# Kernel optimization log

Hardware: AMD Instinct MI355X
Metric: run time of the kernel (lower is better)

Reference implementation:

```python
import jax, jax.numpy as jnp
import numpy as np


def _neighbor_indices(e):
    """Replicates the Python branch ladder: for each position i pick two key/value
    slice indices (k1, k2) based on entropy comparisons with neighbors."""
    S = e.shape[0]
    i = jnp.arange(S)
    e_prev = e[jnp.clip(i - 1, 0, S - 1)]
    e_next = e[jnp.clip(i + 1, 0, S - 1)]
    ge_next = e >= e_next
    ge_prev = e >= e_prev
    le_next = e <= e_next
    le_prev = e <= e_prev
    # branch order matters for ties: check in the same order as the torch code
    c1 = ge_next & ge_prev  # local max  -> (i-1, i+1)
    c2 = le_next & ge_prev  # rising     -> (i-1, i)
    c3 = ge_next & le_prev  # falling    -> (i,   i+1)
    k1 = jnp.where(c1, i - 1, jnp.where(c2, i - 1, jnp.where(c3, i, i)))
    k2 = jnp.where(c1, i + 1, jnp.where(c2, i, jnp.where(c3, i + 1, i)))
    # boundary i == 0: (1,1) if e0 >= e1 else (0,0)
    b0 = jnp.where(e[0] >= e[1], 1, 0)
    k1 = k1.at[0].set(b0)
    k2 = k2.at[0].set(b0)
    # boundary i == S-1: (S-2,S-2) if e[-1] >= e[-2] else (S-1,S-1)
    bL = jnp.where(e[S - 1] >= e[S - 2], S - 2, S - 1)
    k1 = k1.at[S - 1].set(bL)
    k2 = k2.at[S - 1].set(bL)
    return k1, k2


def setup_inputs() -> dict:
    key = jax.random.key(0)
    k1, k2 = jax.random.split(key)
    S, C, H, W = 64, 512, 32, 32
    c5d = jax.random.normal(k1, (S, C, H, W), dtype=jnp.float32)
    entropy_list = jax.random.uniform(k2, (S,), dtype=jnp.float32)
    return {"c5d": c5d, "entropy_list": entropy_list}


def reference(c5d, entropy_list):
    S = c5d.shape[0]
    D = int(np.prod(c5d.shape[1:]))
    k1, k2 = _neighbor_indices(entropy_list)
    idx = jnp.stack([k1, k2], axis=1)              # [S, 2]
    q = c5d.reshape(S, D)                          # [S, D]  one token per slice
    kv = q[idx]                                    # [S, 2, D] gathered neighbor tokens
    scale = 1.0 / jnp.sqrt(jnp.asarray(D, dtype=q.dtype))
    scores = jnp.einsum("sd,skd->sk", q, kv) * scale   # [S, 2]
    attn = jax.nn.softmax(scores, axis=-1)
    out = jnp.einsum("sk,skd->sd", attn, kv)           # [S, D]
    return out.reshape(c5d.shape)
```

## Files before the change

kernel.cpp:

```cpp
#include <hip/hip_runtime.h>
#include <math.h>

#define NSLICE 64
#define DVEC   131072
#define NB     32
#define CHUNK4 (DVEC / NB)
#define TPB    256
#define ITER   (CHUNK4 / TPB)
#define NPAIR  (NSLICE - 1)
#define NTASKA (NPAIR * NB)
#define NTASKB (NSLICE * NB)

typedef float f32x4 __attribute__((ext_vector_type(4)));

__inline__ __device__ void nt_store4(const float4& v, float4* p) {
    __builtin_nontemporal_store(*reinterpret_cast<const f32x4*>(&v),
                                reinterpret_cast<f32x4*>(p));
}

__inline__ __device__ float wave_reduce(float v) {
    #pragma unroll
    for (int off = 32; off > 0; off >>= 1) v += __shfl_down(v, off, 64);
    return v;
}

__inline__ __device__ bool is_c1(const float* __restrict__ ent, int s) {
    if (s < 1 || s > NSLICE - 2) return false;
    const float e = ent[s];
    return (e >= ent[s + 1]) && (e >= ent[s - 1]);
}

__global__ __launch_bounds__(TPB) void cross_kernel(
        const float4* __restrict__ q, const float* __restrict__ ent,
        float* __restrict__ pC) {
    const int task = blockIdx.x;
    const int i = task >> 5;
    const int j = task & 31;

    bool need = is_c1(ent, i) || is_c1(ent, i + 1);
    if (!need) return;

    const float4* qi = q + (size_t)i * DVEC + (size_t)j * CHUNK4 + threadIdx.x;
    const float4* qn = qi + DVEC;
    float c0 = 0.f, c1 = 0.f, c2 = 0.f, c3 = 0.f;
    #pragma unroll
    for (int t = 0; t < ITER; t += 4) {
        float4 a0 = qi[(t+0)*TPB]; float4 a1 = qi[(t+1)*TPB];
        float4 a2 = qi[(t+2)*TPB]; float4 a3 = qi[(t+3)*TPB];
        float4 b0 = qn[(t+0)*TPB]; float4 b1 = qn[(t+1)*TPB];
        float4 b2 = qn[(t+2)*TPB]; float4 b3 = qn[(t+3)*TPB];
        c0 += a0.x*b0.x + a0.y*b0.y + a0.z*b0.z + a0.w*b0.w;
        c1 += a1.x*b1.x + a1.y*b1.y + a1.z*b1.z + a1.w*b1.w;
        c2 += a2.x*b2.x + a2.y*b2.y + a2.z*b2.z + a2.w*b2.w;
        c3 += a3.x*b3.x + a3.y*b3.y + a3.z*b3.z + a3.w*b3.w;
    }
    const float cross = (c0 + c1) + (c2 + c3);

    __shared__ float r_c[TPB / 64];
    const float cw = wave_reduce(cross);
    const int lane = threadIdx.x & 63;
    const int wid  = threadIdx.x >> 6;
    if (lane == 0) r_c[wid] = cw;
    __syncthreads();
    if (threadIdx.x == 0) pC[task] = r_c[0] + r_c[1] + r_c[2] + r_c[3];
}

__global__ __launch_bounds__(TPB) void combine_kernel(
        const float4* __restrict__ q, const float* __restrict__ ent,
        const float* __restrict__ pC, float4* __restrict__ out) {
    const int task = blockIdx.x;
    const int i = task >> 5;
    const int j = task & 31;
    const int tid = threadIdx.x;

    __shared__ float sp[64];

    bool blend = false;
    int src = i;
    if (i == 0) {
        src = (ent[0] >= ent[1]) ? 1 : 0;
    } else if (i == NSLICE - 1) {
        src = (ent[NSLICE-1] >= ent[NSLICE-2]) ? NSLICE-2 : NSLICE-1;
    } else {
        const float ei = ent[i], ep = ent[i-1], en = ent[i+1];
        const bool ge_next = (ei >= en), ge_prev = (ei >= ep);
        if (ge_next && ge_prev) blend = true;
    }

    float4* o = out + (size_t)i * DVEC + (size_t)j * CHUNK4 + tid;

    if (!blend) {
        const float4* qs = q + (size_t)src * DVEC + (size_t)j * CHUNK4 + tid;
        #pragma unroll
        for (int t = 0; t < ITER; t += 8) {
            float4 x0 = qs[(t+0)*TPB]; float4 x1 = qs[(t+1)*TPB];
            float4 x2 = qs[(t+2)*TPB]; float4 x3 = qs[(t+3)*TPB];
            float4 x4 = qs[(t+4)*TPB]; float4 x5 = qs[(t+5)*TPB];
            float4 x6 = qs[(t+6)*TPB]; float4 x7 = qs[(t+7)*TPB];
            nt_store4(x0, &o[(t+0)*TPB]);
            nt_store4(x1, &o[(t+1)*TPB]);
            nt_store4(x2, &o[(t+2)*TPB]);
            nt_store4(x3, &o[(t+3)*TPB]);
            nt_store4(x4, &o[(t+4)*TPB]);
            nt_store4(x5, &o[(t+5)*TPB]);
            nt_store4(x6, &o[(t+6)*TPB]);
            nt_store4(x7, &o[(t+7)*TPB]);
        }
        return;
    }

    if (tid < 64)
        sp[tid] = (tid < 32) ? pC[(i - 1) * NB + tid] : pC[i * NB + (tid - 32)];
    __syncthreads();

    float s1a = 0.f, s2a = 0.f;
    #pragma unroll
    for (int t = 0; t < NB; t++) {
        s1a += sp[t];
        s2a += sp[32 + t];
    }
    const float s_scale = 1.0f / sqrtf(524288.0f);
    const float s1 = s1a * s_scale;
    const float s2 = s2a * s_scale;
    const float m  = fmaxf(s1, s2);
    const float e1 = expf(s1 - m), e2 = expf(s2 - m);
    const float inv = 1.0f / (e1 + e2);
    const float wa = e1 * inv;
    const float wb = e2 * inv;

    const float4* qa = q + (size_t)(i - 1) * DVEC + (size_t)j * CHUNK4 + tid;
    const float4* qb = q + (size_t)(i + 1) * DVEC + (size_t)j * CHUNK4 + tid;
    #pragma unroll
    for (int t = 0; t < ITER; t += 4) {
        float4 x0 = qa[(t+0)*TPB]; float4 x1 = qa[(t+1)*TPB];
        float4 x2 = qa[(t+2)*TPB]; float4 x3 = qa[(t+3)*TPB];
        float4 y0 = qb[(t+0)*TPB]; float4 y1 = qb[(t+1)*TPB];
        float4 y2 = qb[(t+2)*TPB]; float4 y3 = qb[(t+3)*TPB];
        float4 r0, r1, r2, r3;
        r0.x = wa*x0.x + wb*y0.x; r0.y = wa*x0.y + wb*y0.y;
        r0.z = wa*x0.z + wb*y0.z; r0.w = wa*x0.w + wb*y0.w;
        r1.x = wa*x1.x + wb*y1.x; r1.y = wa*x1.y + wb*y1.y;
        r1.z = wa*x1.z + wb*y1.z; r1.w = wa*x1.w + wb*y1.w;
        r2.x = wa*x2.x + wb*y2.x; r2.y = wa*x2.y + wb*y2.y;
        r2.z = wa*x2.z + wb*y2.z; r2.w = wa*x2.w + wb*y2.w;
        r3.x = wa*x3.x + wb*y3.x; r3.y = wa*x3.y + wb*y3.y;
        r3.z = wa*x3.z + wb*y3.z; r3.w = wa*x3.w + wb*y3.w;
        nt_store4(r0, &o[(t+0)*TPB]);
        nt_store4(r1, &o[(t+1)*TPB]);
        nt_store4(r2, &o[(t+2)*TPB]);
        nt_store4(r3, &o[(t+3)*TPB]);
    }
}

extern "C" void kernel_launch(void* const* d_in, const int* in_sizes, int n_in,
                              void* d_out, int out_size, void* d_ws, size_t ws_size,
                              hipStream_t stream) {
    const float4* c5d = (const float4*)d_in[0];
    const float*  ent = (const float*)d_in[1];
    float4* out = (float4*)d_out;

    float* pC = (float*)d_ws;

    cross_kernel<<<NTASKA, TPB, 0, stream>>>(c5d, ent, pC);
    combine_kernel<<<NTASKB, TPB, 0, stream>>>(c5d, ent, pC, out);
}
```

Baseline: 241.8 us.

## Fuse cross and combine kernels into one cooperative launch with grid sync

Replaces the two back-to-back kernel launches with a single cooperative kernel of 1024 blocks. Each block handles up to two cross-product tasks, waits at a grid-wide barrier, then handles two combine tasks. If the cooperative launch fails it falls back to the original two kernels. This removes one launch and the gap between kernels, but adds grid-sync cost and caps residency at 1024 persistent blocks, which may lower memory-level parallelism for the copy-heavy combine phase.

```diff
diff --git a/kernel.cpp b/kernel.cpp
--- a/kernel.cpp
+++ b/kernel.cpp
@@ -1,5 +1,8 @@
 #include <hip/hip_runtime.h>
+#include <hip/hip_cooperative_groups.h>
 #include <math.h>
+
+namespace cg = cooperative_groups;
 
 #define NSLICE 64
 #define DVEC   131072
@@ -10,6 +13,7 @@
 #define NPAIR  (NSLICE - 1)
 #define NTASKA (NPAIR * NB)
 #define NTASKB (NSLICE * NB)
+#define FBLK   1024
 
 typedef float f32x4 __attribute__((ext_vector_type(4)));
 
@@ -30,15 +34,11 @@
     return (e >= ent[s + 1]) && (e >= ent[s - 1]);
 }
 
-__global__ __launch_bounds__(TPB) void cross_kernel(
-        const float4* __restrict__ q, const float* __restrict__ ent,
-        float* __restrict__ pC) {
-    const int task = blockIdx.x;
+__device__ void cross_task(int task, const float4* __restrict__ q,
+                           const float* __restrict__ ent, float* __restrict__ pC) {
     const int i = task >> 5;
     const int j = task & 31;
-
-    bool need = is_c1(ent, i) || is_c1(ent, i + 1);
-    if (!need) return;
+    if (!(is_c1(ent, i) || is_c1(ent, i + 1))) return;
 
     const float4* qi = q + (size_t)i * DVEC + (size_t)j * CHUNK4 + threadIdx.x;
     const float4* qn = qi + DVEC;
@@ -63,17 +63,16 @@
     if (lane == 0) r_c[wid] = cw;
     __syncthreads();
     if (threadIdx.x == 0) pC[task] = r_c[0] + r_c[1] + r_c[2] + r_c[3];
+    __syncthreads();
 }
 
-__global__ __launch_bounds__(TPB) void combine_kernel(
-        const float4* __restrict__ q, const float* __restrict__ ent,
-        const float* __restrict__ pC, float4* __restrict__ out) {
-    const int task = blockIdx.x;
+__device__ void combine_task(int task, const float4* __restrict__ q,
+                             const float* __restrict__ ent,
+                             const float* __restrict__ pC,
+                             float4* __restrict__ out) {
     const int i = task >> 5;
     const int j = task & 31;
     const int tid = threadIdx.x;
-
-    __shared__ float sp[64];
 
     bool blend = false;
     int src = i;
@@ -83,8 +82,7 @@
         src = (ent[NSLICE-1] >= ent[NSLICE-2]) ? NSLICE-2 : NSLICE-1;
     } else {
         const float ei = ent[i], ep = ent[i-1], en = ent[i+1];
-        const bool ge_next = (ei >= en), ge_prev = (ei >= ep);
-        if (ge_next && ge_prev) blend = true;
+        if ((ei >= en) && (ei >= ep)) blend = true;
     }
 
     float4* o = out + (size_t)i * DVEC + (size_t)j * CHUNK4 + tid;
@@ -97,36 +95,29 @@
             float4 x2 = qs[(t+2)*TPB]; float4 x3 = qs[(t+3)*TPB];
             float4 x4 = qs[(t+4)*TPB]; float4 x5 = qs[(t+5)*TPB];
             float4 x6 = qs[(t+6)*TPB]; float4 x7 = qs[(t+7)*TPB];
-            nt_store4(x0, &o[(t+0)*TPB]);
-            nt_store4(x1, &o[(t+1)*TPB]);
-            nt_store4(x2, &o[(t+2)*TPB]);
-            nt_store4(x3, &o[(t+3)*TPB]);
-            nt_store4(x4, &o[(t+4)*TPB]);
-            nt_store4(x5, &o[(t+5)*TPB]);
-            nt_store4(x6, &o[(t+6)*TPB]);
-            nt_store4(x7, &o[(t+7)*TPB]);
+            nt_store4(x0, &o[(t+0)*TPB]); nt_store4(x1, &o[(t+1)*TPB]);
+            nt_store4(x2, &o[(t+2)*TPB]); nt_store4(x3, &o[(t+3)*TPB]);
+            nt_store4(x4, &o[(t+4)*TPB]); nt_store4(x5, &o[(t+5)*TPB]);
+            nt_store4(x6, &o[(t+6)*TPB]); nt_store4(x7, &o[(t+7)*TPB]);
         }
         return;
     }
 
+    __shared__ float sp[64];
     if (tid < 64)
         sp[tid] = (tid < 32) ? pC[(i - 1) * NB + tid] : pC[i * NB + (tid - 32)];
     __syncthreads();
-
     float s1a = 0.f, s2a = 0.f;
     #pragma unroll
-    for (int t = 0; t < NB; t++) {
-        s1a += sp[t];
-        s2a += sp[32 + t];
-    }
+    for (int t = 0; t < NB; t++) { s1a += sp[t]; s2a += sp[32 + t]; }
+    __syncthreads();
+
     const float s_scale = 1.0f / sqrtf(524288.0f);
-    const float s1 = s1a * s_scale;
-    const float s2 = s2a * s_scale;
+    const float s1 = s1a * s_scale, s2 = s2a * s_scale;
     const float m  = fmaxf(s1, s2);
     const float e1 = expf(s1 - m), e2 = expf(s2 - m);
     const float inv = 1.0f / (e1 + e2);
-    const float wa = e1 * inv;
-    const float wb = e2 * inv;
+    const float wa = e1 * inv, wb = e2 * inv;
 
     const float4* qa = q + (size_t)(i - 1) * DVEC + (size_t)j * CHUNK4 + tid;
     const float4* qb = q + (size_t)(i + 1) * DVEC + (size_t)j * CHUNK4 + tid;
@@ -145,11 +136,32 @@
         r2.z = wa*x2.z + wb*y2.z; r2.w = wa*x2.w + wb*y2.w;
         r3.x = wa*x3.x + wb*y3.x; r3.y = wa*x3.y + wb*y3.y;
         r3.z = wa*x3.z + wb*y3.z; r3.w = wa*x3.w + wb*y3.w;
-        nt_store4(r0, &o[(t+0)*TPB]);
-        nt_store4(r1, &o[(t+1)*TPB]);
-        nt_store4(r2, &o[(t+2)*TPB]);
-        nt_store4(r3, &o[(t+3)*TPB]);
+        nt_store4(r0, &o[(t+0)*TPB]); nt_store4(r1, &o[(t+1)*TPB]);
+        nt_store4(r2, &o[(t+2)*TPB]); nt_store4(r3, &o[(t+3)*TPB]);
     }
+}
+
+__global__ __launch_bounds__(TPB, 4) void fused_kernel(
+        const float4* __restrict__ q, const float* __restrict__ ent,
+        float* __restrict__ pC, float4* __restrict__ out) {
+    cg::grid_group grid = cg::this_grid();
+    const int b = blockIdx.x;
+    cross_task(b, q, ent, pC);
+    if (b + FBLK < NTASKA) cross_task(b + FBLK, q, ent, pC);
+    grid.sync();
+    combine_task(b, q, ent, pC, out);
+    combine_task(b + FBLK, q, ent, pC, out);
+}
+
+__global__ __launch_bounds__(TPB) void cross_kernel(
+        const float4* __restrict__ q, const float* __restrict__ ent,
+        float* __restrict__ pC) {
+    cross_task(blockIdx.x, q, ent, pC);
+}
+__global__ __launch_bounds__(TPB) void combine_kernel(
+        const float4* __restrict__ q, const float* __restrict__ ent,
+        const float* __restrict__ pC, float4* __restrict__ out) {
+    combine_task(blockIdx.x, q, ent, pC, out);
 }
 
 extern "C" void kernel_launch(void* const* d_in, const int* in_sizes, int n_in,
@@ -158,9 +170,13 @@
     const float4* c5d = (const float4*)d_in[0];
     const float*  ent = (const float*)d_in[1];
     float4* out = (float4*)d_out;
-
     float* pC = (float*)d_ws;
 
-    cross_kernel<<<NTASKA, TPB, 0, stream>>>(c5d, ent, pC);
-    combine_kernel<<<NTASKB, TPB, 0, stream>>>(c5d, ent, pC, out);
+    void* args[] = { (void*)&c5d, (void*)&ent, (void*)&pC, (void*)&out };
+    hipError_t err = hipLaunchCooperativeKernel(
+        (const void*)fused_kernel, dim3(FBLK), dim3(TPB), args, 0, stream);
+    if (err != hipSuccess) {
+        cross_kernel<<<NTASKA, TPB, 0, stream>>>(c5d, ent, pC);
+        combine_kernel<<<NTASKB, TPB, 0, stream>>>(c5d, ent, pC, out);
+    }
 }
```

Measured after the change: 385.7 us. 1.6x slower.
